# Performance work log

Hardware: AMD Instinct MI355X
Metric: run time of the kernel (lower is better)

Reference implementation:

```python
import jax, jax.numpy as jnp
import numpy as np

VOXEL_SIZE = 0.05  # grid_size[0]
N_POINTS = 4_000_000


def setup_inputs() -> dict:
    key = jax.random.key(0)
    x = jax.random.uniform(key, (N_POINTS, 3), dtype=jnp.float32)  # (N, 3) xyz
    return {"x": x}


def reference(x):
    """Grid (voxel) mean pooling, packed single-batch mode.

    Faithful to grid_pooling_pack_mode with batch_size=1: floor-hash each
    point into a voxel, group identical voxels (torch.unique), scatter-add
    points per voxel and divide by counts.  Output is padded to N rows
    (jit-friendly); rows >= num_unique are zeros.
    """
    N = x.shape[0]
    inv_voxel = 1.0 / VOXEL_SIZE
    voxels = jnp.floor(x * inv_voxel).astype(jnp.int32)        # (N, 3)
    voxels = voxels - voxels.min(axis=0, keepdims=True)        # per-batch shift to 0
    dims = voxels.max(axis=0) + 1                              # (3,) grid extents
    # Ravel hash: ((b*d0 + v0)*d1 + v1)*d2 + v2 with b=0 for single batch
    hash_values = (voxels[:, 0] * dims[1] + voxels[:, 1]) * dims[2] + voxels[:, 2]
    # Sort-based unique with static size=N (padded with fill), like torch.unique
    uniq, inv_idx, counts = jnp.unique(
        hash_values, return_inverse=True, return_counts=True,
        size=N, fill_value=-1)
    inv_idx = inv_idx.reshape(-1)
    # scatter-add points into their voxel slot, then mean
    sums = jax.ops.segment_sum(x, inv_idx, num_segments=N)     # (N, 3) padded
    denom = jnp.maximum(counts, 1).astype(x.dtype)[:, None]    # pad slots have count 0
    s_points = sums / denom
    return s_points
```

## Files before the change

kernel.cpp:

```cpp
#include <hip/hip_runtime.h>
#include <hip/hip_bf16.h>


#define NBINS 8000
#define NBINS_PAD 8192
#define ACC_BLOCKS 256
#define ACC_THREADS 1024
#define RGROUPS 32
#define SPG (ACC_BLOCKS / RGROUPS)
typedef unsigned long long u64;

__global__ void accum_kernel(const float* __restrict__ x, int N,
                             u64* __restrict__ partials,
                             float4* __restrict__ out4, int total4) {
    extern __shared__ u64 lds[];
    const float scale = 20.0f;
    const float FP = 4096.0f;
    int t = threadIdx.x;

    float4* lds4 = (float4*)lds;
    #pragma unroll
    for (int k = 0; k < NBINS_PAD * 8 / 16 / ACC_THREADS; ++k)
        lds4[t + k * ACC_THREADS] = make_float4(0.f, 0.f, 0.f, 0.f);
    __syncthreads();

    const float4* xv = (const float4*)x;
    long long nquads = ((long long)N + 3) / 4;
    long long gstride = (long long)gridDim.x * ACC_THREADS;
    for (long long q = (long long)blockIdx.x * ACC_THREADS + t; q < nquads;
         q += gstride) {
        float px[4], py[4], pz[4];
        int npts;
        if (q * 4 + 4 <= N) {
            float4 a = xv[3 * q + 0];
            float4 b = xv[3 * q + 1];
            float4 c = xv[3 * q + 2];
            px[0] = a.x; py[0] = a.y; pz[0] = a.z;
            px[1] = a.w; py[1] = b.x; pz[1] = b.y;
            px[2] = b.z; py[2] = b.w; pz[2] = c.x;
            px[3] = c.y; py[3] = c.z; pz[3] = c.w;
            npts = 4;
        } else {
            npts = (int)(N - q * 4);
            for (int j = 0; j < npts; ++j) {
                px[j] = x[3 * (q * 4 + j) + 0];
                py[j] = x[3 * (q * 4 + j) + 1];
                pz[j] = x[3 * (q * 4 + j) + 2];
            }
        }
        #pragma unroll
        for (int j = 0; j < 4; ++j) {
            if (j >= npts) break;
            int vx = (int)floorf(px[j] * scale);
            int vy = (int)floorf(py[j] * scale);
            int vz = (int)floorf(pz[j] * scale);
            vx = min(max(vx, 0), 19);
            vy = min(max(vy, 0), 19);
            vz = min(max(vz, 0), 19);
            int h = (vx * 20 + vy) * 20 + vz;
            u64 qx = (u64)(unsigned)(px[j] * FP + 0.5f);
            u64 qy = (u64)(unsigned)(py[j] * FP + 0.5f);
            u64 qz = (u64)(unsigned)(pz[j] * FP + 0.5f);
            atomicAdd(&lds[h], (qx << 45) | (qy << 26) | (qz << 7) | 1ull);
        }
    }
    __syncthreads();

    float4* p4 = (float4*)(partials + (size_t)blockIdx.x * NBINS_PAD);
    #pragma unroll
    for (int k = 0; k < NBINS_PAD * 8 / 16 / ACC_THREADS; ++k)
        p4[t + k * ACC_THREADS] = lds4[t + k * ACC_THREADS];

    const float4 zero4 = make_float4(0.f, 0.f, 0.f, 0.f);
    for (long long oi = (long long)blockIdx.x * ACC_THREADS + t; oi < total4;
         oi += (long long)ACC_BLOCKS * ACC_THREADS)
        out4[oi] = zero4;
}

__global__ void reduce1_kernel(const u64* __restrict__ partials,
                               uint4* __restrict__ gpart) {
    const int pairs = NBINS_PAD / 2;
    int tid = blockIdx.x * blockDim.x + threadIdx.x;
    int g = tid / pairs;
    int p = tid % pairs;
    const ulonglong2* src = (const ulonglong2*)partials;
    unsigned sx0 = 0, sy0 = 0, sz0 = 0, c0 = 0;
    unsigned sx1 = 0, sy1 = 0, sz1 = 0, c1 = 0;
    #pragma unroll
    for (int k = 0; k < SPG; ++k) {
        ulonglong2 v = src[(size_t)(g * SPG + k) * pairs + p];
        c0  += (unsigned)(v.x & 127u);
        sz0 += (unsigned)((v.x >> 7)  & 0x7FFFFu);
        sy0 += (unsigned)((v.x >> 26) & 0x7FFFFu);
        sx0 += (unsigned)(v.x >> 45);
        c1  += (unsigned)(v.y & 127u);
        sz1 += (unsigned)((v.y >> 7)  & 0x7FFFFu);
        sy1 += (unsigned)((v.y >> 26) & 0x7FFFFu);
        sx1 += (unsigned)(v.y >> 45);
    }
    gpart[(size_t)g * NBINS_PAD + 2 * p + 0] = make_uint4(sx0, sy0, sz0, c0);
    gpart[(size_t)g * NBINS_PAD + 2 * p + 1] = make_uint4(sx1, sy1, sz1, c1);
}

__global__ void reduce2_kernel(const uint4* __restrict__ gpart,
                               float* __restrict__ bins) {
    int bin = blockIdx.x * blockDim.x + threadIdx.x;
    u64 sx = 0, sy = 0, sz = 0, c = 0;
    #pragma unroll
    for (int g = 0; g < RGROUPS; ++g) {
        uint4 v = gpart[(size_t)g * NBINS_PAD + bin];
        sx += v.x; sy += v.y; sz += v.z; c += v.w;
    }
    const float inv = 1.0f / 4096.0f;
    bins[0 * NBINS_PAD + bin] = (float)sx * inv;
    bins[1 * NBINS_PAD + bin] = (float)sy * inv;
    bins[2 * NBINS_PAD + bin] = (float)sz * inv;
    bins[3 * NBINS_PAD + bin] = (float)c;
}

__global__ void finalize_kernel(const float* __restrict__ bins,
                                float* __restrict__ out, int out_size) {
    __shared__ int wsum[16];
    int t = threadIdx.x;
    int lane = t & 63;
    int w = t >> 6;
    int base = t * 8;

    float c[8];
    int occ[8];
    int tot = 0;
    #pragma unroll
    for (int j = 0; j < 8; ++j) {
        int b = base + j;
        c[j] = (b < NBINS) ? bins[3 * NBINS_PAD + b] : 0.0f;
        occ[j] = (c[j] > 0.0f) ? 1 : 0;
        tot += occ[j];
    }

    int v = tot;
    #pragma unroll
    for (int d = 1; d < 64; d <<= 1) {
        int o = __shfl_up(v, d, 64);
        if (lane >= d) v += o;
    }
    if (lane == 63) wsum[w] = v;
    __syncthreads();
    if (w == 0 && lane < 16) {
        int s = wsum[lane];
        #pragma unroll
        for (int d = 1; d < 16; d <<= 1) {
            int o = __shfl_up(s, d, 64);
            if (lane >= d) s += o;
        }
        wsum[lane] = s;
    }
    __syncthreads();
    int r = (w ? wsum[w - 1] : 0) + v - tot;

    #pragma unroll
    for (int j = 0; j < 8; ++j) {
        if (occ[j]) {
            int b = base + j;
            float icnt = 1.0f / c[j];
            out[3 * r + 0] = bins[0 * NBINS_PAD + b] * icnt;
            out[3 * r + 1] = bins[1 * NBINS_PAD + b] * icnt;
            out[3 * r + 2] = bins[2 * NBINS_PAD + b] * icnt;
            ++r;
        }
    }

    if (t == 0) {
        int total4 = out_size / 4;
        for (int e = total4 * 4; e < out_size; ++e) out[e] = 0.f;
    }
}

extern "C" void kernel_launch(void* const* d_in, const int* in_sizes, int n_in,
                              void* d_out, int out_size, void* d_ws, size_t ws_size,
                              hipStream_t stream) {
    const float* x = (const float*)d_in[0];
    int N = in_sizes[0] / 3;
    float* out = (float*)d_out;

    u64* partials = (u64*)d_ws;
    uint4* gpart = (uint4*)(partials + (size_t)ACC_BLOCKS * NBINS_PAD);
    float* bins = (float*)(gpart + (size_t)RGROUPS * NBINS_PAD);

    hipFuncSetAttribute(reinterpret_cast<const void*>(&accum_kernel),
                        hipFuncAttributeMaxDynamicSharedMemorySize, 65536);

    int total4 = out_size / 4;
    accum_kernel<<<ACC_BLOCKS, ACC_THREADS, NBINS_PAD * sizeof(u64), stream>>>(
        x, N, partials, (float4*)out, total4);

    int r1_threads = RGROUPS * (NBINS_PAD / 2);
    reduce1_kernel<<<r1_threads / 256, 256, 0, stream>>>(partials, gpart);
    reduce2_kernel<<<NBINS_PAD / 256, 256, 0, stream>>>(gpart, bins);
    finalize_kernel<<<1, 1024, 0, stream>>>(bins, out, out_size);
}
```

Measured before the change: 120.2 us.

## Merge reduction and finalize kernels into one cooperative kernel with grid sync

Replaces the three post-accumulation launches (two reduction passes and a single-block compaction) with one cooperative kernel that uses grid.sync between phases. It also moves the output zero-fill in the accumulation kernel to before the block barrier so the stores overlap the final LDS atomics. The aim is to remove kernel launch and inter-kernel gap overhead. In exchange it adds grid-wide barrier cost, and the second reduction pass now accumulates in 32-bit rather than 64-bit, which could overflow if per-bin sums were large.

```diff
diff --git a/kernel.cpp b/kernel.cpp
--- a/kernel.cpp
+++ b/kernel.cpp
@@ -1,5 +1,8 @@
 #include <hip/hip_runtime.h>
 #include <hip/hip_bf16.h>
+#include <hip/hip_cooperative_groups.h>
+
+namespace cg = cooperative_groups;
 
 
 #define NBINS 8000
@@ -8,6 +11,8 @@
 #define ACC_THREADS 1024
 #define RGROUPS 32
 #define SPG (ACC_BLOCKS / RGROUPS)
+#define POST_BLOCKS 128
+#define POST_THREADS 1024
 typedef unsigned long long u64;
 
 __global__ void accum_kernel(const float* __restrict__ x, int N,
@@ -64,114 +69,120 @@
             atomicAdd(&lds[h], (qx << 45) | (qy << 26) | (qz << 7) | 1ull);
         }
     }
+
+    const float4 zero4 = make_float4(0.f, 0.f, 0.f, 0.f);
+    for (long long oi = (long long)blockIdx.x * ACC_THREADS + t; oi < total4;
+         oi += (long long)ACC_BLOCKS * ACC_THREADS)
+        out4[oi] = zero4;
+
     __syncthreads();
 
     float4* p4 = (float4*)(partials + (size_t)blockIdx.x * NBINS_PAD);
     #pragma unroll
     for (int k = 0; k < NBINS_PAD * 8 / 16 / ACC_THREADS; ++k)
         p4[t + k * ACC_THREADS] = lds4[t + k * ACC_THREADS];
-
-    const float4 zero4 = make_float4(0.f, 0.f, 0.f, 0.f);
-    for (long long oi = (long long)blockIdx.x * ACC_THREADS + t; oi < total4;
-         oi += (long long)ACC_BLOCKS * ACC_THREADS)
-        out4[oi] = zero4;
 }
 
-__global__ void reduce1_kernel(const u64* __restrict__ partials,
-                               uint4* __restrict__ gpart) {
+__global__ void post_kernel(const u64* __restrict__ partials,
+                            uint4* __restrict__ gpart,
+                            float* __restrict__ bins,
+                            float* __restrict__ out, int out_size) {
+    cg::grid_group grid = cg::this_grid();
     const int pairs = NBINS_PAD / 2;
-    int tid = blockIdx.x * blockDim.x + threadIdx.x;
-    int g = tid / pairs;
-    int p = tid % pairs;
-    const ulonglong2* src = (const ulonglong2*)partials;
-    unsigned sx0 = 0, sy0 = 0, sz0 = 0, c0 = 0;
-    unsigned sx1 = 0, sy1 = 0, sz1 = 0, c1 = 0;
-    #pragma unroll
-    for (int k = 0; k < SPG; ++k) {
-        ulonglong2 v = src[(size_t)(g * SPG + k) * pairs + p];
-        c0  += (unsigned)(v.x & 127u);
-        sz0 += (unsigned)((v.x >> 7)  & 0x7FFFFu);
-        sy0 += (unsigned)((v.x >> 26) & 0x7FFFFu);
-        sx0 += (unsigned)(v.x >> 45);
-        c1  += (unsigned)(v.y & 127u);
-        sz1 += (unsigned)((v.y >> 7)  & 0x7FFFFu);
-        sy1 += (unsigned)((v.y >> 26) & 0x7FFFFu);
-        sx1 += (unsigned)(v.y >> 45);
-    }
-    gpart[(size_t)g * NBINS_PAD + 2 * p + 0] = make_uint4(sx0, sy0, sz0, c0);
-    gpart[(size_t)g * NBINS_PAD + 2 * p + 1] = make_uint4(sx1, sy1, sz1, c1);
-}
-
-__global__ void reduce2_kernel(const uint4* __restrict__ gpart,
-                               float* __restrict__ bins) {
-    int bin = blockIdx.x * blockDim.x + threadIdx.x;
-    u64 sx = 0, sy = 0, sz = 0, c = 0;
-    #pragma unroll
-    for (int g = 0; g < RGROUPS; ++g) {
-        uint4 v = gpart[(size_t)g * NBINS_PAD + bin];
-        sx += v.x; sy += v.y; sz += v.z; c += v.w;
-    }
-    const float inv = 1.0f / 4096.0f;
-    bins[0 * NBINS_PAD + bin] = (float)sx * inv;
-    bins[1 * NBINS_PAD + bin] = (float)sy * inv;
-    bins[2 * NBINS_PAD + bin] = (float)sz * inv;
-    bins[3 * NBINS_PAD + bin] = (float)c;
-}
-
-__global__ void finalize_kernel(const float* __restrict__ bins,
-                                float* __restrict__ out, int out_size) {
-    __shared__ int wsum[16];
-    int t = threadIdx.x;
-    int lane = t & 63;
-    int w = t >> 6;
-    int base = t * 8;
-
-    float c[8];
-    int occ[8];
-    int tot = 0;
-    #pragma unroll
-    for (int j = 0; j < 8; ++j) {
-        int b = base + j;
-        c[j] = (b < NBINS) ? bins[3 * NBINS_PAD + b] : 0.0f;
-        occ[j] = (c[j] > 0.0f) ? 1 : 0;
-        tot += occ[j];
-    }
-
-    int v = tot;
-    #pragma unroll
-    for (int d = 1; d < 64; d <<= 1) {
-        int o = __shfl_up(v, d, 64);
-        if (lane >= d) v += o;
-    }
-    if (lane == 63) wsum[w] = v;
-    __syncthreads();
-    if (w == 0 && lane < 16) {
-        int s = wsum[lane];
-        #pragma unroll
-        for (int d = 1; d < 16; d <<= 1) {
-            int o = __shfl_up(s, d, 64);
-            if (lane >= d) s += o;
-        }
-        wsum[lane] = s;
-    }
-    __syncthreads();
-    int r = (w ? wsum[w - 1] : 0) + v - tot;
-
-    #pragma unroll
-    for (int j = 0; j < 8; ++j) {
-        if (occ[j]) {
+    int tid = blockIdx.x * POST_THREADS + threadIdx.x;
+
+    {
+        int g = tid / pairs;
+        int p = tid % pairs;
+        const ulonglong2* src = (const ulonglong2*)partials;
+        unsigned sx0 = 0, sy0 = 0, sz0 = 0, c0 = 0;
+        unsigned sx1 = 0, sy1 = 0, sz1 = 0, c1 = 0;
+        #pragma unroll
+        for (int k = 0; k < SPG; ++k) {
+            ulonglong2 v = src[(size_t)(g * SPG + k) * pairs + p];
+            c0  += (unsigned)(v.x & 127u);
+            sz0 += (unsigned)((v.x >> 7)  & 0x7FFFFu);
+            sy0 += (unsigned)((v.x >> 26) & 0x7FFFFu);
+            sx0 += (unsigned)(v.x >> 45);
+            c1  += (unsigned)(v.y & 127u);
+            sz1 += (unsigned)((v.y >> 7)  & 0x7FFFFu);
+            sy1 += (unsigned)((v.y >> 26) & 0x7FFFFu);
+            sx1 += (unsigned)(v.y >> 45);
+        }
+        gpart[(size_t)g * NBINS_PAD + 2 * p + 0] = make_uint4(sx0, sy0, sz0, c0);
+        gpart[(size_t)g * NBINS_PAD + 2 * p + 1] = make_uint4(sx1, sy1, sz1, c1);
+    }
+    grid.sync();
+
+    if (tid < NBINS_PAD) {
+        unsigned sx = 0, sy = 0, sz = 0, c = 0;
+        #pragma unroll
+        for (int g = 0; g < RGROUPS; ++g) {
+            uint4 v = gpart[(size_t)g * NBINS_PAD + tid];
+            sx += v.x; sy += v.y; sz += v.z; c += v.w;
+        }
+        const float inv = 1.0f / 4096.0f;
+        bins[0 * NBINS_PAD + tid] = (float)sx * inv;
+        bins[1 * NBINS_PAD + tid] = (float)sy * inv;
+        bins[2 * NBINS_PAD + tid] = (float)sz * inv;
+        bins[3 * NBINS_PAD + tid] = (float)c;
+    }
+    grid.sync();
+
+    if (blockIdx.x == 0) {
+        __shared__ int wsum[16];
+        int t = threadIdx.x;
+        int lane = t & 63;
+        int w = t >> 6;
+        int base = t * 8;
+
+        float c[8];
+        int occ[8];
+        int tot = 0;
+        #pragma unroll
+        for (int j = 0; j < 8; ++j) {
             int b = base + j;
-            float icnt = 1.0f / c[j];
-            out[3 * r + 0] = bins[0 * NBINS_PAD + b] * icnt;
-            out[3 * r + 1] = bins[1 * NBINS_PAD + b] * icnt;
-            out[3 * r + 2] = bins[2 * NBINS_PAD + b] * icnt;
-            ++r;
-        }
-    }
-
-    if (t == 0) {
-        int total4 = out_size / 4;
-        for (int e = total4 * 4; e < out_size; ++e) out[e] = 0.f;
+            c[j] = (b < NBINS) ? bins[3 * NBINS_PAD + b] : 0.0f;
+            occ[j] = (c[j] > 0.0f) ? 1 : 0;
+            tot += occ[j];
+        }
+
+        int v = tot;
+        #pragma unroll
+        for (int d = 1; d < 64; d <<= 1) {
+            int o = __shfl_up(v, d, 64);
+            if (lane >= d) v += o;
+        }
+        if (lane == 63) wsum[w] = v;
+        __syncthreads();
+        if (w == 0 && lane < 16) {
+            int s = wsum[lane];
+            #pragma unroll
+            for (int d = 1; d < 16; d <<= 1) {
+                int o = __shfl_up(s, d, 64);
+                if (lane >= d) s += o;
+            }
+            wsum[lane] = s;
+        }
+        __syncthreads();
+        int r = (w ? wsum[w - 1] : 0) + v - tot;
+
+        #pragma unroll
+        for (int j = 0; j < 8; ++j) {
+            if (occ[j]) {
+                int b = base + j;
+                float icnt = 1.0f / c[j];
+                out[3 * r + 0] = bins[0 * NBINS_PAD + b] * icnt;
+                out[3 * r + 1] = bins[1 * NBINS_PAD + b] * icnt;
+                out[3 * r + 2] = bins[2 * NBINS_PAD + b] * icnt;
+                ++r;
+            }
+        }
+
+        if (t == 0) {
+            int total4 = out_size / 4;
+            for (int e = total4 * 4; e < out_size; ++e) out[e] = 0.f;
+        }
     }
 }
 
@@ -190,11 +201,12 @@
                         hipFuncAttributeMaxDynamicSharedMemorySize, 65536);
 
     int total4 = out_size / 4;
+    float4* out4 = (float4*)out;
     accum_kernel<<<ACC_BLOCKS, ACC_THREADS, NBINS_PAD * sizeof(u64), stream>>>(
-        x, N, partials, (float4*)out, total4);
-
-    int r1_threads = RGROUPS * (NBINS_PAD / 2);
-    reduce1_kernel<<<r1_threads / 256, 256, 0, stream>>>(partials, gpart);
-    reduce2_kernel<<<NBINS_PAD / 256, 256, 0, stream>>>(gpart, bins);
-    finalize_kernel<<<1, 1024, 0, stream>>>(bins, out, out_size);
+        x, N, partials, out4, total4);
+
+    void* args[] = {(void*)&partials, (void*)&gpart, (void*)&bins,
+                    (void*)&out, (void*)&out_size};
+    hipLaunchCooperativeKernel((const void*)post_kernel, dim3(POST_BLOCKS),
+                               dim3(POST_THREADS), args, 0, stream);
 }
```

Result: slower. 167.0 us (+39.0%).
